# Kernel optimization log

Hardware: AMD Instinct MI355X
Metric: run time of the kernel (lower is better)

## Reference

```python
import jax, jax.numpy as jnp
import numpy as np

B, N, D = 32, 2048, 128
HALF = D // 2
DT = 0.01  # interval = [0.0, 0.01], euler solver -> single step of size 0.01


def setup_inputs() -> dict:
    key = jax.random.key(0)
    ks = jax.random.split(key, 10)
    x = jax.random.normal(ks[0], (B, N, D), dtype=jnp.float32)
    hz = jax.random.normal(ks[1], (B, N, D), dtype=jnp.float32)
    # row-normalized random adjacency so adj @ h stays O(1) (avoids tanh saturation)
    adj = jax.random.uniform(ks[2], (N, N), dtype=jnp.float32) / N
    W1 = jax.random.normal(ks[3], (D, D), dtype=jnp.float32) * 0.05
    W2 = jax.random.normal(ks[4], (D, D), dtype=jnp.float32) * 0.05
    Wa = jax.random.normal(ks[5], (2 * D, 2 * D), dtype=jnp.float32) * 0.05
    ba = jnp.zeros((2 * D,), dtype=jnp.float32)
    Wb = jax.random.normal(ks[6], (2 * D, D), dtype=jnp.float32) * 0.05
    bb = jnp.zeros((D,), dtype=jnp.float32)
    # nn.Parameter init is zeros in torch; randomize in [0,0.1] for a nontrivial baseline
    eps = jax.random.uniform(ks[7], (B, N, HALF), dtype=jnp.float32) * 0.1
    return {"x": x, "hz": hz, "adj": adj, "W1": W1, "W2": W2,
            "Wa": Wa, "ba": ba, "Wb": Wb, "bb": bb, "eps": eps}


def reference(x, hz, adj, W1, W2, Wa, ba, Wb, bb, eps):
    # MLP gating: Linear(2D,2D) -> ReLU -> Linear(2D,D) -> Tanh
    u = jnp.concatenate([x, hz], axis=-1)            # [B,N,2D]
    h = jnp.tanh(jax.nn.relu(u @ Wa + ba) @ Wb + bb)  # [B,N,D]

    def gnn_func(h, W):
        # f(t, h) = tanh(A @ h @ W)  (graph diffusion ODE func)
        return jnp.tanh(jnp.einsum('nm,bmd->bnd', adj, h) @ W)

    def euler_step(h, W):
        # odeint(euler, t=[0, 0.01]): one step y1 = y0 + dt * f(0, y0)
        return h + DT * gnn_func(h, W)

    eps_c = jnp.clip(eps, 0.0, 0.1)
    for _ in range(2):
        h_f = euler_step(h, W1)[..., :HALF]                      # [B,N,D/2]
        h = jnp.concatenate([h_f, h[..., HALF:]], axis=-1)       # [B,N,D]
        h_s = eps_c * euler_step(h, W2)[..., HALF:]              # [B,N,D/2]
        h = jnp.concatenate([h_f, h_s], axis=-1)                 # [B,N,D]
    return h
```

## Files before the change

### kernel.cpp

```cpp
#include <hip/hip_runtime.h>


typedef unsigned short u16;
typedef unsigned int   u32;
typedef unsigned long long u64;
typedef __attribute__((ext_vector_type(8))) short bf8;
typedef __attribute__((ext_vector_type(4))) float f4;

#define AS1 __attribute__((address_space(1)))
#define AS3 __attribute__((address_space(3)))

__device__ __forceinline__ void gl_lds16(const void* g, void* l) {
  __builtin_amdgcn_global_load_lds((const AS1 u32*)g, (AS3 u32*)l, 16, 0, 0);
}
__device__ __forceinline__ float bf2f(u16 v) {
  u32 u = ((u32)v) << 16; return __builtin_bit_cast(float, u);
}
__device__ __forceinline__ u16 f2bf(float f) {
  u32 u = __builtin_bit_cast(u32, f);
  return (u16)((u + 0x7fffu + ((u >> 16) & 1u)) >> 16);
}
__device__ __forceinline__ float ldf(const void* p, size_t i, u32 isf32) {
  return isf32 ? ((const float*)p)[i] : bf2f(((const u16*)p)[i]);
}

__device__ __forceinline__ void stage128x32(const u16* grow0, int stride, u16* lds,
                                            int wave, int lane) {
  int r0 = wave * 16 + (lane >> 2);
  int c0 = (lane & 3) * 8;
  gl_lds16(grow0 + (size_t)r0 * stride + c0, lds + wave * 512);
  gl_lds16(grow0 + (size_t)(64 + r0) * stride + c0, lds + 2048 + wave * 512);
}
__device__ __forceinline__ void stage64x32(const u16* grow0, int stride, u16* lds,
                                           int wave, int lane) {
  gl_lds16(grow0 + (size_t)(wave * 16 + (lane >> 2)) * stride + (lane & 3) * 8,
           lds + wave * 512);
}

__global__ void detect_dtype(const u16* __restrict__ x_raw, u32* __restrict__ flag) {
  __shared__ int s;
  int tid = threadIdx.x;
  if (tid == 0) s = 0;
  __syncthreads();
  int huge = 0;
#pragma unroll
  for (int j = 0; j < 16; ++j) {
    u16 v = x_raw[tid * 16 + j];
    u32 e = (v >> 7) & 0xFF;
    if (e >= 0xC0) huge = 1;
  }
  if (huge) atomicOr(&s, 1);
  __syncthreads();
  if (tid == 0) flag[0] = (u32)s;
}

__global__ void cvt_bf16(const void* __restrict__ in, u16* __restrict__ out,
                         long in_off, int n, const u32* __restrict__ flag) {
  u32 isf32 = flag[0];
  int gid = blockIdx.x * 256 + threadIdx.x;
  long i = in_off + (long)gid * 4;
  if (gid * 4 >= n) return;
  u16 o0, o1, o2, o3;
  if (isf32) {
    f4 v = *(const f4*)&((const float*)in)[i];
    o0 = f2bf(v[0]); o1 = f2bf(v[1]); o2 = f2bf(v[2]); o3 = f2bf(v[3]);
  } else {
    u64 v = *(const u64*)&((const u16*)in)[i];
    o0 = (u16)v; o1 = (u16)(v >> 16); o2 = (u16)(v >> 32); o3 = (u16)(v >> 48);
  }
  u64 pk = (u64)o0 | ((u64)o1 << 16) | ((u64)o2 << 32) | ((u64)o3 << 48);
  *(u64*)&out[(size_t)gid * 4] = pk;
}

__global__ void prep_weights(const void* __restrict__ Wa, const void* __restrict__ Wb,
                             const void* __restrict__ W1, const void* __restrict__ W2,
                             u16* __restrict__ WaT, u16* __restrict__ WbT,
                             u16* __restrict__ W1T, u16* __restrict__ W2T,
                             const u32* __restrict__ flag) {
  u32 isf32 = flag[0];
  int i = blockIdx.x * 256 + threadIdx.x;
  if (i < 65536) {
    int o = i >> 8, k = i & 255; WaT[o * 256 + k] = f2bf(ldf(Wa, (size_t)k * 256 + o, isf32));
  } else if (i < 98304) {
    int j = i - 65536; int o = j >> 8, k = j & 255;
    WbT[o * 256 + k] = f2bf(ldf(Wb, (size_t)k * 128 + o, isf32));
  } else if (i < 106496) {
    int j = i - 98304; int jj = j >> 7, k = j & 127;
    W1T[jj * 128 + k] = f2bf(ldf(W1, (size_t)k * 128 + jj, isf32));
  } else {
    int j = i - 106496; int jj = j >> 7, k = j & 127;
    W2T[jj * 128 + k] = f2bf(ldf(W2, (size_t)k * 128 + 64 + jj, isf32));
  }
}

__global__ __launch_bounds__(256, 2) void mlp_fused(const void* __restrict__ x,
                                                    const void* __restrict__ hz,
                                                    const u16* __restrict__ WaT,
                                                    const void* __restrict__ ba,
                                                    const u16* __restrict__ WbT,
                                                    const void* __restrict__ bb,
                                                    const u16* __restrict__ W1T,
                                                    u16* __restrict__ hT,
                                                    u16* __restrict__ hW,
                                                    const u32* __restrict__ flag) {
  __shared__ __align__(16) u16 Z[64 * 264];
  __shared__ __align__(16) u16 pool[10240];
  u16* lA = pool;
  u16* lB = pool + 2048;
  u16* hN = pool;
  u32 isf32 = flag[0];
  int tid = threadIdx.x, lane = tid & 63, wave = tid >> 6;
  int col = lane & 15, quad = lane >> 4;
  int r0 = blockIdx.x * 64;
  int b = r0 >> 11;

  f4 acc[4][4] = {};
  for (int kk = 0; kk < 8; ++kk) {
    int k0 = kk * 32;
    const void* src = (kk < 4) ? x : hz;
    int csrc = (kk < 4) ? k0 : (k0 - 128);
    __syncthreads();
    {
      int row = tid >> 2, c0 = (tid & 3) * 8;
      size_t g = (size_t)(r0 + row) * 128 + csrc + c0;
      uint4 pk;
      if (isf32) {
        f4 v0 = *(const f4*)&((const float*)src)[g];
        f4 v1 = *(const f4*)&((const float*)src)[g + 4];
        pk.x = (u32)f2bf(v0[0]) | ((u32)f2bf(v0[1]) << 16);
        pk.y = (u32)f2bf(v0[2]) | ((u32)f2bf(v0[3]) << 16);
        pk.z = (u32)f2bf(v1[0]) | ((u32)f2bf(v1[1]) << 16);
        pk.w = (u32)f2bf(v1[2]) | ((u32)f2bf(v1[3]) << 16);
      } else {
        pk = *(const uint4*)&((const u16*)src)[g];
      }
      *(uint4*)&lA[row * 32 + c0] = pk;
    }
    stage128x32(WaT + k0, 256, lB, wave, lane);
    stage128x32(WaT + (size_t)128 * 256 + k0, 256, lB + 4096, wave, lane);
    __syncthreads();
    bf8 af[4], bfr[4];
#pragma unroll
    for (int mi = 0; mi < 4; ++mi) af[mi] = *(const bf8*)&lA[(mi * 16 + col) * 32 + quad * 8];
#pragma unroll
    for (int nj = 0; nj < 4; ++nj) bfr[nj] = *(const bf8*)&lB[(wave * 64 + nj * 16 + col) * 32 + quad * 8];
#pragma unroll
    for (int mi = 0; mi < 4; ++mi)
#pragma unroll
      for (int nj = 0; nj < 4; ++nj)
        acc[mi][nj] = __builtin_amdgcn_mfma_f32_16x16x32_bf16(af[mi], bfr[nj], acc[mi][nj], 0, 0, 0);
  }
#pragma unroll
  for (int mi = 0; mi < 4; ++mi)
#pragma unroll
    for (int nj = 0; nj < 4; ++nj) {
      int o = wave * 64 + nj * 16 + col;
      float bav = ldf(ba, o, isf32);
      int rl = mi * 16 + quad * 4;
#pragma unroll
      for (int r = 0; r < 4; ++r)
        Z[(rl + r) * 264 + o] = f2bf(fmaxf(acc[mi][nj][r] + bav, 0.f));
    }
  __syncthreads();

  f4 acc2[4][2] = {};
  for (int kk = 0; kk < 8; ++kk) {
    int k0 = kk * 32;
    if (kk) __syncthreads();
    stage128x32(WbT + k0, 256, lB, wave, lane);
    __syncthreads();
    bf8 az[4], bw[2];
#pragma unroll
    for (int mi = 0; mi < 4; ++mi) az[mi] = *(const bf8*)&Z[(mi * 16 + col) * 264 + k0 + quad * 8];
#pragma unroll
    for (int nj = 0; nj < 2; ++nj) bw[nj] = *(const bf8*)&lB[(wave * 32 + nj * 16 + col) * 32 + quad * 8];
#pragma unroll
    for (int mi = 0; mi < 4; ++mi)
#pragma unroll
      for (int nj = 0; nj < 2; ++nj)
        acc2[mi][nj] = __builtin_amdgcn_mfma_f32_16x16x32_bf16(az[mi], bw[nj], acc2[mi][nj], 0, 0, 0);
  }
  __syncthreads();

#pragma unroll
  for (int mi = 0; mi < 4; ++mi)
#pragma unroll
    for (int nj = 0; nj < 2; ++nj) {
      int d = wave * 32 + nj * 16 + col;
      float bbv = ldf(bb, d, isf32);
      int rl = mi * 16 + quad * 4;
      int rabs = r0 + rl;
      int n = rabs & 2047;
      u16 p[4];
#pragma unroll
      for (int r = 0; r < 4; ++r) {
        p[r] = f2bf(tanhf(acc2[mi][nj][r] + bbv));
        hN[(rl + r) * 136 + d] = p[r];
      }
      u64 pk = (u64)p[0] | ((u64)p[1] << 16) | ((u64)p[2] << 32) | ((u64)p[3] << 48);
      *(u64*)&hT[(size_t)(b * 128 + d) * 2048 + n] = pk;
    }
  __syncthreads();

  f4 acc3[4] = {};
#pragma unroll
  for (int ks = 0; ks < 4; ++ks) {
    bf8 aw[4], bg;
#pragma unroll
    for (int mi = 0; mi < 4; ++mi)
      aw[mi] = *(const bf8*)&W1T[(size_t)(mi * 16 + col) * 128 + ks * 32 + quad * 8];
    bg = *(const bf8*)&hN[(wave * 16 + col) * 136 + ks * 32 + quad * 8];
#pragma unroll
    for (int mi = 0; mi < 4; ++mi)
      acc3[mi] = __builtin_amdgcn_mfma_f32_16x16x32_bf16(aw[mi], bg, acc3[mi], 0, 0, 0);
  }
#pragma unroll
  for (int mi = 0; mi < 4; ++mi) {
    int rloc = wave * 16 + col;
    int ng = (r0 & 2047) + rloc;
#pragma unroll
    for (int r = 0; r < 4; ++r) {
      int j = mi * 16 + quad * 4 + r;
      hW[(size_t)(b * 64 + j) * 2048 + ng] = f2bf(acc3[mi][r]);
    }
  }
}

__global__ __launch_bounds__(256, 2) void fused_step2(const u16* __restrict__ hin,
                                                      const u16* __restrict__ hWT,
                                                      const u16* __restrict__ adjb,
                                                      const u16* __restrict__ WnT,
                                                      const void* __restrict__ eps,
                                                      u16* __restrict__ hout,
                                                      u16* __restrict__ hWout,
                                                      int half, const u32* __restrict__ flag) {
  __shared__ __align__(16) u16 smem[24576];
  u16* lA = smem;
  u16* lB = smem + 8192;
  u16* gN = smem;
  u32 isf32 = flag[0];
  int tid = threadIdx.x, lane = tid & 63, wave = tid >> 6;
  int col = lane & 15, quad = lane >> 4;
  int b = blockIdx.y;
  int n0 = blockIdx.x * 128;

  const u16* Arow = hWT + (size_t)(b * 64) * 2048;
  const u16* Brow = adjb + (size_t)n0 * 2048;

  f4 acc[4][2] = {};
  for (int kk = 0; kk < 16; ++kk) {
    int k0 = kk * 128;
#pragma unroll
    for (int p = 0; p < 4; ++p) {
      stage64x32(Arow + k0 + p * 32, 2048, lA + p * 2048, wave, lane);
      stage128x32(Brow + k0 + p * 32, 2048, lB + p * 4096, wave, lane);
    }
    __syncthreads();
#pragma unroll
    for (int p = 0; p < 4; ++p) {
      bf8 af[4], bfr[2];
#pragma unroll
      for (int mi = 0; mi < 4; ++mi) af[mi] = *(const bf8*)&lA[p * 2048 + (mi * 16 + col) * 32 + quad * 8];
#pragma unroll
      for (int nj = 0; nj < 2; ++nj) bfr[nj] = *(const bf8*)&lB[p * 4096 + (wave * 32 + nj * 16 + col) * 32 + quad * 8];
#pragma unroll
      for (int mi = 0; mi < 4; ++mi)
#pragma unroll
        for (int nj = 0; nj < 2; ++nj)
          acc[mi][nj] = __builtin_amdgcn_mfma_f32_16x16x32_bf16(af[mi], bfr[nj], acc[mi][nj], 0, 0, 0);
    }
    __syncthreads();
  }

  bool has_eps = (eps != nullptr);
  bool mk_hw = (WnT != nullptr);
  int dBase = half * 64;
#pragma unroll
  for (int mi = 0; mi < 4; ++mi)
#pragma unroll
    for (int nj = 0; nj < 2; ++nj) {
      int j0 = mi * 16 + quad * 4;
      int nl = wave * 32 + nj * 16 + col;
      int n = n0 + nl;
      float ev[4];
      if (has_eps) {
        size_t eoff = ((size_t)b * 2048 + n) * 64 + j0;
        if (isf32) {
          f4 e = *(const f4*)&((const float*)eps)[eoff];
          ev[0] = e[0]; ev[1] = e[1]; ev[2] = e[2]; ev[3] = e[3];
        } else {
          u64 e = *(const u64*)&((const u16*)eps)[eoff];
          ev[0] = bf2f((u16)e); ev[1] = bf2f((u16)(e >> 16));
          ev[2] = bf2f((u16)(e >> 32)); ev[3] = bf2f((u16)(e >> 48));
        }
      }
      u16 pv[4];
#pragma unroll
      for (int r = 0; r < 4; ++r) {
        int j = j0 + r;
        size_t idx = (size_t)(b * 128 + dBase + j) * 2048 + n;
        float hold = bf2f(hin[idx]);
        float nh = hold + 0.01f * tanhf(acc[mi][nj][r]);
        if (has_eps) {
          float e = fminf(fmaxf(ev[r], 0.f), 0.1f);
          nh = e * nh;
        }
        pv[r] = f2bf(nh);
        hout[idx] = pv[r];
      }
      if (mk_hw) {
        u64 pk = (u64)pv[0] | ((u64)pv[1] << 16) | ((u64)pv[2] << 32) | ((u64)pv[3] << 48);
        *(u64*)&gN[nl * 136 + dBase + j0] = pk;
      }
    }

  {
    int oh = (1 - half) * 64;
    const u16* src = hin + (size_t)(b * 128 + oh) * 2048 + n0;
    u16* dst = hout + (size_t)(b * 128 + oh) * 2048 + n0;
#pragma unroll
    for (int i = 0; i < 4; ++i) {
      int idx = i * 256 + tid;
      int rr = idx >> 4;
      int cc = (idx & 15) * 8;
      uint4 v = *(const uint4*)&src[(size_t)rr * 2048 + cc];
      *(uint4*)&dst[(size_t)rr * 2048 + cc] = v;
      if (mk_hw) {
        u16 t[8];
        *(uint4*)t = v;
#pragma unroll
        for (int q = 0; q < 8; ++q) gN[(cc + q) * 136 + oh + rr] = t[q];
      }
    }
  }

  if (mk_hw) {
    __syncthreads();
    f4 acc2[4][2] = {};
#pragma unroll
    for (int ks = 0; ks < 4; ++ks) {
      bf8 aw[4], bg[2];
#pragma unroll
      for (int mi = 0; mi < 4; ++mi)
        aw[mi] = *(const bf8*)&WnT[(size_t)(mi * 16 + col) * 128 + ks * 32 + quad * 8];
#pragma unroll
      for (int nj = 0; nj < 2; ++nj)
        bg[nj] = *(const bf8*)&gN[(wave * 32 + nj * 16 + col) * 136 + ks * 32 + quad * 8];
#pragma unroll
      for (int mi = 0; mi < 4; ++mi)
#pragma unroll
        for (int nj = 0; nj < 2; ++nj)
          acc2[mi][nj] = __builtin_amdgcn_mfma_f32_16x16x32_bf16(aw[mi], bg[nj], acc2[mi][nj], 0, 0, 0);
    }
#pragma unroll
    for (int mi = 0; mi < 4; ++mi)
#pragma unroll
      for (int nj = 0; nj < 2; ++nj) {
        int jp0 = mi * 16 + quad * 4;
        int n = n0 + wave * 32 + nj * 16 + col;
#pragma unroll
        for (int r = 0; r < 4; ++r)
          hWout[(size_t)(b * 64 + jp0 + r) * 2048 + n] = f2bf(acc2[mi][nj][r]);
      }
  }
}

__global__ void untranspose(const u16* __restrict__ hT, void* __restrict__ out,
                            const u32* __restrict__ flag) {
  __shared__ __align__(16) u16 t[64][65];
  u32 isf32 = flag[0];
  int b = blockIdx.z, d0 = blockIdx.y * 64, n0 = blockIdx.x * 64;
  int tid = threadIdx.x;
#pragma unroll
  for (int i = 0; i < 16; ++i) {
    int idx = tid + i * 256;
    int r = idx >> 6, c = idx & 63;
    t[r][c] = hT[(size_t)(b * 128 + d0 + r) * 2048 + n0 + c];
  }
  __syncthreads();
#pragma unroll
  for (int i = 0; i < 16; ++i) {
    int idx = tid + i * 256;
    int r = idx >> 6, c = idx & 63;
    size_t o = (size_t)(b * 2048 + n0 + r) * 128 + d0 + c;
    if (isf32) ((float*)out)[o] = bf2f(t[c][r]);
    else       ((u16*)out)[o] = t[c][r];
  }
}

extern "C" void kernel_launch(void* const* d_in, const int* in_sizes, int n_in,
                              void* d_out, int out_size, void* d_ws, size_t ws_size,
                              hipStream_t stream) {
  const void* x   = d_in[0];
  const void* hz  = d_in[1];
  const void* adj = d_in[2];
  const void* W1  = d_in[3];
  const void* W2  = d_in[4];
  const void* Wa  = d_in[5];
  const void* ba  = d_in[6];
  const void* Wb  = d_in[7];
  const void* bb  = d_in[8];
  const void* eps = d_in[9];

  char* ws = (char*)d_ws;
  u16* hA   = (u16*)(ws);
  u16* adjb = (u16*)(ws + (17ull << 20));
  u16* hWa  = (u16*)(ws + (26ull << 20));
  u16* hWb  = (u16*)(ws + (35ull << 20));
  u16* WaT  = (u16*)(ws + (44ull << 20));
  u16* WbT  = WaT + 256 * 256;
  u16* W1T  = WbT + 128 * 256;
  u16* W2T  = W1T + 64 * 128;
  u32* flag = (u32*)(W2T + 64 * 128);
  u16* hB   = (u16*)d_out;

  detect_dtype<<<dim3(1), dim3(256), 0, stream>>>((const u16*)x, flag);
  prep_weights<<<dim3(448), dim3(256), 0, stream>>>(Wa, Wb, W1, W2, WaT, WbT, W1T, W2T, flag);
  cvt_bf16<<<dim3(4096), dim3(256), 0, stream>>>(adj, adjb, 0, 4194304, flag);
  mlp_fused<<<dim3(1024), dim3(256), 0, stream>>>(x, hz, WaT, ba, WbT, bb, W1T, hA, hWa, flag);
  fused_step2<<<dim3(16, 32), dim3(256), 0, stream>>>(hA, hWa, adjb, W2T, nullptr, hB, hWb, 0, flag);
  fused_step2<<<dim3(16, 32), dim3(256), 0, stream>>>(hB, hWb, adjb, W1T, eps, hA, hWa, 1, flag);
  fused_step2<<<dim3(16, 32), dim3(256), 0, stream>>>(hA, hWa, adjb, W2T, nullptr, hB, hWb, 0, flag);
  fused_step2<<<dim3(16, 32), dim3(256), 0, stream>>>(hB, hWb, adjb, nullptr, eps, hA, nullptr, 1, flag);
  untranspose<<<dim3(32, 2, 32), dim3(256), 0, stream>>>(hA, d_out, flag);
}
```

Baseline: 348.2 us.

## Double-buffer LDS staging and switch to conflict-free quad-major tile layout

Converts the GEMM main loops in mlp_fused and fused_step2 to double-buffered LDS staging, issuing the next tile's global-to-LDS loads before the current tile's MFMAs so that loads overlap compute and one barrier per iteration is removed. It also changes the staged tile layout to a quad-major arrangement (row within 16 contiguous per k-quad) so MFMA fragment reads from LDS avoid bank conflicts. The fused_step2 K-step shrinks from 128 to 64 to fit two buffers, and mlp_fused's LDS pool doubles. The cost is higher LDS use, which may affect occupancy, and more barriers per unit of K in fused_step2.

```diff
diff --git a/kernel.cpp b/kernel.cpp
--- a/kernel.cpp
+++ b/kernel.cpp
@@ -24,17 +24,16 @@
   return isf32 ? ((const float*)p)[i] : bf2f(((const u16*)p)[i]);
 }
 
-__device__ __forceinline__ void stage128x32(const u16* grow0, int stride, u16* lds,
+__device__ __forceinline__ void stage64x32q(const u16* g, int stride, u16* lds,
                                             int wave, int lane) {
-  int r0 = wave * 16 + (lane >> 2);
-  int c0 = (lane & 3) * 8;
-  gl_lds16(grow0 + (size_t)r0 * stride + c0, lds + wave * 512);
-  gl_lds16(grow0 + (size_t)(64 + r0) * stride + c0, lds + 2048 + wave * 512);
-}
-__device__ __forceinline__ void stage64x32(const u16* grow0, int stride, u16* lds,
-                                           int wave, int lane) {
-  gl_lds16(grow0 + (size_t)(wave * 16 + (lane >> 2)) * stride + (lane & 3) * 8,
+  gl_lds16(g + (size_t)(wave * 16 + (lane & 15)) * stride + (lane >> 4) * 8,
            lds + wave * 512);
+}
+__device__ __forceinline__ void stage128x32q(const u16* g, int stride, u16* lds,
+                                             int wave, int lane) {
+  int r = lane & 15, qk = (lane >> 4) * 8;
+  gl_lds16(g + (size_t)(wave * 16 + r) * stride + qk, lds + wave * 512);
+  gl_lds16(g + (size_t)((wave + 4) * 16 + r) * stride + qk, lds + (wave + 4) * 512);
 }
 
 __global__ void detect_dtype(const u16* __restrict__ x_raw, u32* __restrict__ flag) {
@@ -104,9 +103,7 @@
                                                     u16* __restrict__ hW,
                                                     const u32* __restrict__ flag) {
   __shared__ __align__(16) u16 Z[64 * 264];
-  __shared__ __align__(16) u16 pool[10240];
-  u16* lA = pool;
-  u16* lB = pool + 2048;
+  __shared__ __align__(16) u16 pool[20480];
   u16* hN = pool;
   u32 isf32 = flag[0];
   int tid = threadIdx.x, lane = tid & 63, wave = tid >> 6;
@@ -114,42 +111,74 @@
   int r0 = blockIdx.x * 64;
   int b = r0 >> 11;
 
-  f4 acc[4][4] = {};
-  for (int kk = 0; kk < 8; ++kk) {
+  struct A2 { uint4 a, b; };
+  auto loadA = [&](int kk) -> A2 {
     int k0 = kk * 32;
     const void* src = (kk < 4) ? x : hz;
     int csrc = (kk < 4) ? k0 : (k0 - 128);
-    __syncthreads();
-    {
-      int row = tid >> 2, c0 = (tid & 3) * 8;
-      size_t g = (size_t)(r0 + row) * 128 + csrc + c0;
-      uint4 pk;
-      if (isf32) {
-        f4 v0 = *(const f4*)&((const float*)src)[g];
-        f4 v1 = *(const f4*)&((const float*)src)[g + 4];
-        pk.x = (u32)f2bf(v0[0]) | ((u32)f2bf(v0[1]) << 16);
-        pk.y = (u32)f2bf(v0[2]) | ((u32)f2bf(v0[3]) << 16);
-        pk.z = (u32)f2bf(v1[0]) | ((u32)f2bf(v1[1]) << 16);
-        pk.w = (u32)f2bf(v1[2]) | ((u32)f2bf(v1[3]) << 16);
-      } else {
-        pk = *(const uint4*)&((const u16*)src)[g];
-      }
-      *(uint4*)&lA[row * 32 + c0] = pk;
-    }
-    stage128x32(WaT + k0, 256, lB, wave, lane);
-    stage128x32(WaT + (size_t)128 * 256 + k0, 256, lB + 4096, wave, lane);
-    __syncthreads();
+    int row = tid >> 2, c0 = (tid & 3) * 8;
+    size_t g = (size_t)(r0 + row) * 128 + csrc + c0;
+    A2 v;
+    if (isf32) {
+      v.a = *(const uint4*)&((const float*)src)[g];
+      v.b = *(const uint4*)&((const float*)src)[g + 4];
+    } else {
+      v.a = *(const uint4*)&((const u16*)src)[g];
+    }
+    return v;
+  };
+  auto writeA = [&](int buf, A2 v) {
+    uint4 pk;
+    if (isf32) {
+      f4 v0 = __builtin_bit_cast(f4, v.a), v1 = __builtin_bit_cast(f4, v.b);
+      pk.x = (u32)f2bf(v0[0]) | ((u32)f2bf(v0[1]) << 16);
+      pk.y = (u32)f2bf(v0[2]) | ((u32)f2bf(v0[3]) << 16);
+      pk.z = (u32)f2bf(v1[0]) | ((u32)f2bf(v1[1]) << 16);
+      pk.w = (u32)f2bf(v1[2]) | ((u32)f2bf(v1[3]) << 16);
+    } else {
+      pk = v.a;
+    }
+    int row = tid >> 2;
+    *(uint4*)&pool[buf * 2048 + (row >> 4) * 512 + (tid & 3) * 128 + (row & 15) * 8] = pk;
+  };
+  auto stageB1 = [&](int buf, int kk) {
+    int k0 = kk * 32;
+    u16* lb = pool + 4096 + buf * 8192;
+    stage128x32q(WaT + k0, 256, lb, wave, lane);
+    stage128x32q(WaT + (size_t)128 * 256 + k0, 256, lb + 4096, wave, lane);
+  };
+
+  f4 acc[4][4] = {};
+  {
+    A2 v0 = loadA(0);
+    stageB1(0, 0);
+    writeA(0, v0);
+  }
+  __syncthreads();
+  for (int kk = 0; kk < 8; ++kk) {
+    int cur = kk & 1;
+    A2 nx;
+    if (kk < 7) { nx = loadA(kk + 1); stageB1(cur ^ 1, kk + 1); }
+    const u16* la = pool + cur * 2048;
+    const u16* lb = pool + 4096 + cur * 8192;
     bf8 af[4], bfr[4];
 #pragma unroll
-    for (int mi = 0; mi < 4; ++mi) af[mi] = *(const bf8*)&lA[(mi * 16 + col) * 32 + quad * 8];
-#pragma unroll
-    for (int nj = 0; nj < 4; ++nj) bfr[nj] = *(const bf8*)&lB[(wave * 64 + nj * 16 + col) * 32 + quad * 8];
+    for (int mi = 0; mi < 4; ++mi) af[mi] = *(const bf8*)&la[mi * 512 + quad * 128 + col * 8];
+#pragma unroll
+    for (int nj = 0; nj < 4; ++nj) bfr[nj] = *(const bf8*)&lb[(wave * 4 + nj) * 512 + quad * 128 + col * 8];
 #pragma unroll
     for (int mi = 0; mi < 4; ++mi)
 #pragma unroll
       for (int nj = 0; nj < 4; ++nj)
         acc[mi][nj] = __builtin_amdgcn_mfma_f32_16x16x32_bf16(af[mi], bfr[nj], acc[mi][nj], 0, 0, 0);
-  }
+    if (kk < 7) writeA(cur ^ 1, nx);
+    __syncthreads();
+  }
+
+  auto stageB2 = [&](int buf, int kk) {
+    stage128x32q(WbT + kk * 32, 256, pool + 4096 + buf * 4096, wave, lane);
+  };
+  stageB2(0, 0);
 #pragma unroll
   for (int mi = 0; mi < 4; ++mi)
 #pragma unroll
@@ -165,22 +194,22 @@
 
   f4 acc2[4][2] = {};
   for (int kk = 0; kk < 8; ++kk) {
+    int cur = kk & 1;
+    if (kk < 7) stageB2(cur ^ 1, kk + 1);
     int k0 = kk * 32;
-    if (kk) __syncthreads();
-    stage128x32(WbT + k0, 256, lB, wave, lane);
-    __syncthreads();
+    const u16* lb = pool + 4096 + cur * 4096;
     bf8 az[4], bw[2];
 #pragma unroll
     for (int mi = 0; mi < 4; ++mi) az[mi] = *(const bf8*)&Z[(mi * 16 + col) * 264 + k0 + quad * 8];
 #pragma unroll
-    for (int nj = 0; nj < 2; ++nj) bw[nj] = *(const bf8*)&lB[(wave * 32 + nj * 16 + col) * 32 + quad * 8];
+    for (int nj = 0; nj < 2; ++nj) bw[nj] = *(const bf8*)&lb[(wave * 2 + nj) * 512 + quad * 128 + col * 8];
 #pragma unroll
     for (int mi = 0; mi < 4; ++mi)
 #pragma unroll
       for (int nj = 0; nj < 2; ++nj)
         acc2[mi][nj] = __builtin_amdgcn_mfma_f32_16x16x32_bf16(az[mi], bw[nj], acc2[mi][nj], 0, 0, 0);
-  }
-  __syncthreads();
+    __syncthreads();
+  }
 
 #pragma unroll
   for (int mi = 0; mi < 4; ++mi)
@@ -235,8 +264,6 @@
                                                       u16* __restrict__ hWout,
                                                       int half, const u32* __restrict__ flag) {
   __shared__ __align__(16) u16 smem[24576];
-  u16* lA = smem;
-  u16* lB = smem + 8192;
   u16* gN = smem;
   u32 isf32 = flag[0];
   int tid = threadIdx.x, lane = tid & 63, wave = tid >> 6;
@@ -247,22 +274,36 @@
   const u16* Arow = hWT + (size_t)(b * 64) * 2048;
   const u16* Brow = adjb + (size_t)n0 * 2048;
 
+  auto STAGE = [&](int buf, int t) {
+    int k0 = t * 64;
+    u16* la = smem + buf * 4096;
+    u16* lb = smem + 8192 + buf * 8192;
+#pragma unroll
+    for (int p = 0; p < 2; ++p) {
+      int kp = k0 + p * 32;
+      stage64x32q(Arow + kp, 2048, la + p * 2048, wave, lane);
+      stage128x32q(Brow + kp, 2048, lb + p * 4096, wave, lane);
+    }
+  };
+
   f4 acc[4][2] = {};
-  for (int kk = 0; kk < 16; ++kk) {
-    int k0 = kk * 128;
-#pragma unroll
-    for (int p = 0; p < 4; ++p) {
-      stage64x32(Arow + k0 + p * 32, 2048, lA + p * 2048, wave, lane);
-      stage128x32(Brow + k0 + p * 32, 2048, lB + p * 4096, wave, lane);
-    }
-    __syncthreads();
-#pragma unroll
-    for (int p = 0; p < 4; ++p) {
+  STAGE(0, 0);
+  __syncthreads();
+#pragma unroll 2
+  for (int kk = 0; kk < 32; ++kk) {
+    int cur = kk & 1;
+    if (kk < 31) STAGE(cur ^ 1, kk + 1);
+    const u16* la = smem + cur * 4096;
+    const u16* lb = smem + 8192 + cur * 8192;
+#pragma unroll
+    for (int p = 0; p < 2; ++p) {
       bf8 af[4], bfr[2];
 #pragma unroll
-      for (int mi = 0; mi < 4; ++mi) af[mi] = *(const bf8*)&lA[p * 2048 + (mi * 16 + col) * 32 + quad * 8];
-#pragma unroll
-      for (int nj = 0; nj < 2; ++nj) bfr[nj] = *(const bf8*)&lB[p * 4096 + (wave * 32 + nj * 16 + col) * 32 + quad * 8];
+      for (int mi = 0; mi < 4; ++mi)
+        af[mi] = *(const bf8*)&la[p * 2048 + mi * 512 + quad * 128 + col * 8];
+#pragma unroll
+      for (int nj = 0; nj < 2; ++nj)
+        bfr[nj] = *(const bf8*)&lb[p * 4096 + (wave * 2 + nj) * 512 + quad * 128 + col * 8];
 #pragma unroll
       for (int mi = 0; mi < 4; ++mi)
 #pragma unroll
```

New measurement: 443.7 us. 27.4% more time.

## Triple-buffer async LDS staging with vmcnt waits in MLP and graph GEMM kernels

Applied to the files above, without the earlier changes.

Replaces the load-then-compute loops in mlp_fused and fused_step2 with a three-stage ring of LDS buffers. Global-to-LDS loads are issued two steps ahead and gated by s_waitcnt vmcnt plus a raw barrier, and MFMA sections are raised with s_setprio. The activation tile is preloaded whole, and staging switches to a quad-major LDS layout. This is meant to hide global memory latency behind MFMA work, at the cost of more LDS per block, which may lower occupancy, and fragile hand-counted wait values.

```diff
diff --git a/kernel.cpp b/kernel.cpp
--- a/kernel.cpp
+++ b/kernel.cpp
@@ -9,6 +9,8 @@
 
 #define AS1 __attribute__((address_space(1)))
 #define AS3 __attribute__((address_space(3)))
+#define WAITVM(N) asm volatile("s_waitcnt vmcnt(" #N ")" ::: "memory")
+#define BARS __builtin_amdgcn_s_barrier()
 
 __device__ __forceinline__ void gl_lds16(const void* g, void* l) {
   __builtin_amdgcn_global_load_lds((const AS1 u32*)g, (AS3 u32*)l, 16, 0, 0);
@@ -24,17 +26,16 @@
   return isf32 ? ((const float*)p)[i] : bf2f(((const u16*)p)[i]);
 }
 
-__device__ __forceinline__ void stage128x32(const u16* grow0, int stride, u16* lds,
+__device__ __forceinline__ void stage64x32q(const u16* g, int stride, u16* lds,
                                             int wave, int lane) {
-  int r0 = wave * 16 + (lane >> 2);
-  int c0 = (lane & 3) * 8;
-  gl_lds16(grow0 + (size_t)r0 * stride + c0, lds + wave * 512);
-  gl_lds16(grow0 + (size_t)(64 + r0) * stride + c0, lds + 2048 + wave * 512);
-}
-__device__ __forceinline__ void stage64x32(const u16* grow0, int stride, u16* lds,
-                                           int wave, int lane) {
-  gl_lds16(grow0 + (size_t)(wave * 16 + (lane >> 2)) * stride + (lane & 3) * 8,
+  gl_lds16(g + (size_t)(wave * 16 + (lane & 15)) * stride + (lane >> 4) * 8,
            lds + wave * 512);
+}
+__device__ __forceinline__ void stage128x32q(const u16* g, int stride, u16* lds,
+                                             int wave, int lane) {
+  int r = lane & 15, qk = (lane >> 4) * 8;
+  gl_lds16(g + (size_t)(wave * 16 + r) * stride + qk, lds + wave * 512);
+  gl_lds16(g + (size_t)((wave + 4) * 16 + r) * stride + qk, lds + (wave + 4) * 512);
 }
 
 __global__ void detect_dtype(const u16* __restrict__ x_raw, u32* __restrict__ flag) {
@@ -103,26 +104,53 @@
                                                     u16* __restrict__ hT,
                                                     u16* __restrict__ hW,
                                                     const u32* __restrict__ flag) {
-  __shared__ __align__(16) u16 Z[64 * 264];
-  __shared__ __align__(16) u16 pool[10240];
-  u16* lA = pool;
-  u16* lB = pool + 2048;
-  u16* hN = pool;
+  __shared__ __align__(16) u16 smem[40960];
+  u16* Afull = smem;
+  u16* Zp = smem + 16384;
+  u16* hN = smem;
   u32 isf32 = flag[0];
   int tid = threadIdx.x, lane = tid & 63, wave = tid >> 6;
   int col = lane & 15, quad = lane >> 4;
   int r0 = blockIdx.x * 64;
   int b = r0 >> 11;
 
+  auto stageB1 = [&](int buf, int kk) {
+    u16* lb = smem + 16384 + buf * 8192;
+    stage128x32q(WaT + kk * 32, 256, lb, wave, lane);
+    stage128x32q(WaT + (size_t)128 * 256 + kk * 32, 256, lb + 4096, wave, lane);
+  };
+  auto stageB2 = [&](int buf, int kk) {
+    stage128x32q(WbT + kk * 32, 256, smem + buf * 4096, wave, lane);
+  };
+
   f4 acc[4][4] = {};
-  for (int kk = 0; kk < 8; ++kk) {
-    int k0 = kk * 32;
-    const void* src = (kk < 4) ? x : hz;
-    int csrc = (kk < 4) ? k0 : (k0 - 128);
-    __syncthreads();
-    {
-      int row = tid >> 2, c0 = (tid & 3) * 8;
-      size_t g = (size_t)(r0 + row) * 128 + csrc + c0;
+  auto P1 = [&](int buf, int kk) {
+    const u16* lb = smem + 16384 + buf * 8192;
+    bf8 af[4], bfr[4];
+#pragma unroll
+    for (int mi = 0; mi < 4; ++mi)
+      af[mi] = *(const bf8*)&Afull[kk * 2048 + mi * 512 + quad * 128 + col * 8];
+#pragma unroll
+    for (int nj = 0; nj < 4; ++nj)
+      bfr[nj] = *(const bf8*)&lb[(wave * 4 + nj) * 512 + quad * 128 + col * 8];
+    __builtin_amdgcn_s_setprio(1);
+#pragma unroll
+    for (int mi = 0; mi < 4; ++mi)
+#pragma unroll
+      for (int nj = 0; nj < 4; ++nj)
+        acc[mi][nj] = __builtin_amdgcn_mfma_f32_16x16x32_bf16(af[mi], bfr[nj], acc[mi][nj], 0, 0, 0);
+    __builtin_amdgcn_s_setprio(0);
+  };
+
+  stageB1(0, 0); stageB1(1, 1);
+  {
+    int r = ((tid >> 6) << 4) | (tid & 15);
+    int c0 = ((tid >> 4) & 3) * 8;
+#pragma unroll
+    for (int kk = 0; kk < 8; ++kk) {
+      const void* src = (kk < 4) ? x : hz;
+      int cc = (kk & 3) * 32 + c0;
+      size_t g = (size_t)(r0 + r) * 128 + cc;
       uint4 pk;
       if (isf32) {
         f4 v0 = *(const f4*)&((const float*)src)[g];
@@ -134,22 +162,22 @@
       } else {
         pk = *(const uint4*)&((const u16*)src)[g];
       }
-      *(uint4*)&lA[row * 32 + c0] = pk;
-    }
-    stage128x32(WaT + k0, 256, lB, wave, lane);
-    stage128x32(WaT + (size_t)128 * 256 + k0, 256, lB + 4096, wave, lane);
-    __syncthreads();
-    bf8 af[4], bfr[4];
-#pragma unroll
-    for (int mi = 0; mi < 4; ++mi) af[mi] = *(const bf8*)&lA[(mi * 16 + col) * 32 + quad * 8];
-#pragma unroll
-    for (int nj = 0; nj < 4; ++nj) bfr[nj] = *(const bf8*)&lB[(wave * 64 + nj * 16 + col) * 32 + quad * 8];
-#pragma unroll
-    for (int mi = 0; mi < 4; ++mi)
-#pragma unroll
-      for (int nj = 0; nj < 4; ++nj)
-        acc[mi][nj] = __builtin_amdgcn_mfma_f32_16x16x32_bf16(af[mi], bfr[nj], acc[mi][nj], 0, 0, 0);
-  }
+      *(uint4*)&Afull[kk * 2048 + tid * 8] = pk;
+    }
+  }
+  __syncthreads();
+
+#pragma unroll 1
+  for (int kk0 = 0; kk0 < 6; kk0 += 3) {
+    WAITVM(4); BARS; stageB1(2, kk0 + 2); P1(0, kk0);
+    WAITVM(4); BARS; stageB1(0, kk0 + 3); P1(1, kk0 + 1);
+    WAITVM(4); BARS; stageB1(1, kk0 + 4); P1(2, kk0 + 2);
+  }
+  WAITVM(4); BARS; P1(0, 6);
+  WAITVM(0); BARS; P1(1, 7);
+  __syncthreads();
+
+  stageB2(0, 0); stageB2(1, 1);
 #pragma unroll
   for (int mi = 0; mi < 4; ++mi)
 #pragma unroll
@@ -159,27 +187,37 @@
       int rl = mi * 16 + quad * 4;
 #pragma unroll
       for (int r = 0; r < 4; ++r)
-        Z[(rl + r) * 264 + o] = f2bf(fmaxf(acc[mi][nj][r] + bav, 0.f));
-    }
-  __syncthreads();
+        Zp[(rl + r) * 264 + o] = f2bf(fmaxf(acc[mi][nj][r] + bav, 0.f));
+    }
+  asm volatile("s_waitcnt lgkmcnt(0)" ::: "memory");
+  BARS;
 
   f4 acc2[4][2] = {};
-  for (int kk = 0; kk < 8; ++kk) {
-    int k0 = kk * 32;
-    if (kk) __syncthreads();
-    stage128x32(WbT + k0, 256, lB, wave, lane);
-    __syncthreads();
+  auto P2 = [&](int buf, int kk) {
+    const u16* lb = smem + buf * 4096;
     bf8 az[4], bw[2];
 #pragma unroll
-    for (int mi = 0; mi < 4; ++mi) az[mi] = *(const bf8*)&Z[(mi * 16 + col) * 264 + k0 + quad * 8];
-#pragma unroll
-    for (int nj = 0; nj < 2; ++nj) bw[nj] = *(const bf8*)&lB[(wave * 32 + nj * 16 + col) * 32 + quad * 8];
+    for (int mi = 0; mi < 4; ++mi)
+      az[mi] = *(const bf8*)&Zp[(mi * 16 + col) * 264 + kk * 32 + quad * 8];
+#pragma unroll
+    for (int nj = 0; nj < 2; ++nj)
+      bw[nj] = *(const bf8*)&lb[(wave * 2 + nj) * 512 + quad * 128 + col * 8];
+    __builtin_amdgcn_s_setprio(1);
 #pragma unroll
     for (int mi = 0; mi < 4; ++mi)
 #pragma unroll
       for (int nj = 0; nj < 2; ++nj)
         acc2[mi][nj] = __builtin_amdgcn_mfma_f32_16x16x32_bf16(az[mi], bw[nj], acc2[mi][nj], 0, 0, 0);
-  }
+    __builtin_amdgcn_s_setprio(0);
+  };
+#pragma unroll 1
+  for (int kk0 = 0; kk0 < 6; kk0 += 3) {
+    WAITVM(2); BARS; stageB2(2, kk0 + 2); P2(0, kk0);
+    WAITVM(2); BARS; stageB2(0, kk0 + 3); P2(1, kk0 + 1);
+    WAITVM(2); BARS; stageB2(1, kk0 + 4); P2(2, kk0 + 2);
+  }
+  WAITVM(2); BARS; P2(0, 6);
+  WAITVM(0); BARS; P2(1, 7);
   __syncthreads();
 
 #pragma unroll
@@ -234,9 +272,7 @@
                                                       u16* __restrict__ hout,
                                                       u16* __restrict__ hWout,
                                                       int half, const u32* __restrict__ flag) {
-  __shared__ __align__(16) u16 smem[24576];
-  u16* lA = smem;
-  u16* lB = smem + 8192;
+  __shared__ __align__(16) u16 smem[36864];
   u16* gN = smem;
   u32 isf32 = flag[0];
   int tid = threadIdx.x, lane = tid & 63, wave = tid >> 6;
@@ -247,30 +283,52 @@
   const u16* Arow = hWT + (size_t)(b * 64) * 2048;
   const u16* Brow = adjb + (size_t)n0 * 2048;
 
+  auto STAGE = [&](int buf, int t) {
+    int k0 = t * 64;
+    u16* la = smem + buf * 12288;
+    u16* lb = la + 4096;
+#pragma unroll
+    for (int p = 0; p < 2; ++p) {
+      stage64x32q(Arow + k0 + p * 32, 2048, la + p * 2048, wave, lane);
+      stage128x32q(Brow + k0 + p * 32, 2048, lb + p * 4096, wave, lane);
+    }
+  };
+
   f4 acc[4][2] = {};
-  for (int kk = 0; kk < 16; ++kk) {
-    int k0 = kk * 128;
-#pragma unroll
-    for (int p = 0; p < 4; ++p) {
-      stage64x32(Arow + k0 + p * 32, 2048, lA + p * 2048, wave, lane);
-      stage128x32(Brow + k0 + p * 32, 2048, lB + p * 4096, wave, lane);
-    }
-    __syncthreads();
-#pragma unroll
-    for (int p = 0; p < 4; ++p) {
-      bf8 af[4], bfr[2];
-#pragma unroll
-      for (int mi = 0; mi < 4; ++mi) af[mi] = *(const bf8*)&lA[p * 2048 + (mi * 16 + col) * 32 + quad * 8];
-#pragma unroll
-      for (int nj = 0; nj < 2; ++nj) bfr[nj] = *(const bf8*)&lB[p * 4096 + (wave * 32 + nj * 16 + col) * 32 + quad * 8];
+  auto COMP = [&](int buf) {
+    const u16* la = smem + buf * 12288;
+    const u16* lb = la + 4096;
+    bf8 af[2][4], bfr[2][2];
+#pragma unroll
+    for (int p = 0; p < 2; ++p) {
 #pragma unroll
       for (int mi = 0; mi < 4; ++mi)
+        af[p][mi] = *(const bf8*)&la[p * 2048 + mi * 512 + quad * 128 + col * 8];
+#pragma unroll
+      for (int nj = 0; nj < 2; ++nj)
+        bfr[p][nj] = *(const bf8*)&lb[p * 4096 + (wave * 2 + nj) * 512 + quad * 128 + col * 8];
+    }
+    __builtin_amdgcn_s_setprio(1);
+#pragma unroll
+    for (int p = 0; p < 2; ++p)
+#pragma unroll
+      for (int mi = 0; mi < 4; ++mi)
 #pragma unroll
         for (int nj = 0; nj < 2; ++nj)
-          acc[mi][nj] = __builtin_amdgcn_mfma_f32_16x16x32_bf16(af[mi], bfr[nj], acc[mi][nj], 0, 0, 0);
-    }
-    __syncthreads();
-  }
+          acc[mi][nj] = __builtin_amdgcn_mfma_f32_16x16x32_bf16(af[p][mi], bfr[p][nj], acc[mi][nj], 0, 0, 0);
+    __builtin_amdgcn_s_setprio(0);
+  };
+
+  STAGE(0, 0); STAGE(1, 1);
+#pragma unroll 1
+  for (int kk0 = 0; kk0 < 30; kk0 += 3) {
+    WAITVM(6); BARS; STAGE(2, kk0 + 2); COMP(0);
+    WAITVM(6); BARS; STAGE(0, kk0 + 3); COMP(1);
+    WAITVM(6); BARS; STAGE(1, kk0 + 4); COMP(2);
+  }
+  WAITVM(6); BARS; COMP(0);
+  WAITVM(0); BARS; COMP(1);
+  __syncthreads();
 
   bool has_eps = (eps != nullptr);
   bool mk_hw = (WnT != nullptr);
```

New measurement: 432.5 us. 1.24x slower.

## Load GEMM operands directly from global into registers with register double-buffering

Applied to the files above, without the earlier changes.

Drops LDS staging through global_load_lds in the adjacency GEMM and the MLP weight GEMMs. MFMA fragments are now loaded straight from global memory into registers, with a two-deep software pipeline and no block barriers in the main loops. The grid order is swapped so consecutive blocks share the adjacency rows via L2, and launch bounds are raised to 4 blocks per SM for occupancy. The cost is that each wave now issues its own uncoalesced 16-byte row loads, with no cross-wave sharing of A and B tiles, which raises L2 traffic.

```diff
diff --git a/kernel.cpp b/kernel.cpp
--- a/kernel.cpp
+++ b/kernel.cpp
@@ -7,12 +7,6 @@
 typedef __attribute__((ext_vector_type(8))) short bf8;
 typedef __attribute__((ext_vector_type(4))) float f4;
 
-#define AS1 __attribute__((address_space(1)))
-#define AS3 __attribute__((address_space(3)))
-
-__device__ __forceinline__ void gl_lds16(const void* g, void* l) {
-  __builtin_amdgcn_global_load_lds((const AS1 u32*)g, (AS3 u32*)l, 16, 0, 0);
-}
 __device__ __forceinline__ float bf2f(u16 v) {
   u32 u = ((u32)v) << 16; return __builtin_bit_cast(float, u);
 }
@@ -22,19 +16,6 @@
 }
 __device__ __forceinline__ float ldf(const void* p, size_t i, u32 isf32) {
   return isf32 ? ((const float*)p)[i] : bf2f(((const u16*)p)[i]);
-}
-
-__device__ __forceinline__ void stage128x32(const u16* grow0, int stride, u16* lds,
-                                            int wave, int lane) {
-  int r0 = wave * 16 + (lane >> 2);
-  int c0 = (lane & 3) * 8;
-  gl_lds16(grow0 + (size_t)r0 * stride + c0, lds + wave * 512);
-  gl_lds16(grow0 + (size_t)(64 + r0) * stride + c0, lds + 2048 + wave * 512);
-}
-__device__ __forceinline__ void stage64x32(const u16* grow0, int stride, u16* lds,
-                                           int wave, int lane) {
-  gl_lds16(grow0 + (size_t)(wave * 16 + (lane >> 2)) * stride + (lane & 3) * 8,
-           lds + wave * 512);
 }
 
 __global__ void detect_dtype(const u16* __restrict__ x_raw, u32* __restrict__ flag) {
@@ -103,26 +84,23 @@
                                                     u16* __restrict__ hT,
                                                     u16* __restrict__ hW,
                                                     const u32* __restrict__ flag) {
+  __shared__ __align__(16) u16 Afull[16384];
   __shared__ __align__(16) u16 Z[64 * 264];
-  __shared__ __align__(16) u16 pool[10240];
-  u16* lA = pool;
-  u16* lB = pool + 2048;
-  u16* hN = pool;
+  u16* hN = Afull;
   u32 isf32 = flag[0];
   int tid = threadIdx.x, lane = tid & 63, wave = tid >> 6;
   int col = lane & 15, quad = lane >> 4;
   int r0 = blockIdx.x * 64;
   int b = r0 >> 11;
 
-  f4 acc[4][4] = {};
-  for (int kk = 0; kk < 8; ++kk) {
-    int k0 = kk * 32;
-    const void* src = (kk < 4) ? x : hz;
-    int csrc = (kk < 4) ? k0 : (k0 - 128);
-    __syncthreads();
-    {
-      int row = tid >> 2, c0 = (tid & 3) * 8;
-      size_t g = (size_t)(r0 + row) * 128 + csrc + c0;
+  {
+    int r = ((tid >> 6) << 4) | (tid & 15);
+    int c0 = ((tid >> 4) & 3) * 8;
+#pragma unroll
+    for (int kk = 0; kk < 8; ++kk) {
+      const void* src = (kk < 4) ? x : hz;
+      int cc = (kk & 3) * 32 + c0;
+      size_t g = (size_t)(r0 + r) * 128 + cc;
       uint4 pk;
       if (isf32) {
         f4 v0 = *(const f4*)&((const float*)src)[g];
@@ -134,21 +112,38 @@
       } else {
         pk = *(const uint4*)&((const u16*)src)[g];
       }
-      *(uint4*)&lA[row * 32 + c0] = pk;
-    }
-    stage128x32(WaT + k0, 256, lB, wave, lane);
-    stage128x32(WaT + (size_t)128 * 256 + k0, 256, lB + 4096, wave, lane);
-    __syncthreads();
-    bf8 af[4], bfr[4];
-#pragma unroll
-    for (int mi = 0; mi < 4; ++mi) af[mi] = *(const bf8*)&lA[(mi * 16 + col) * 32 + quad * 8];
-#pragma unroll
-    for (int nj = 0; nj < 4; ++nj) bfr[nj] = *(const bf8*)&lB[(wave * 64 + nj * 16 + col) * 32 + quad * 8];
-#pragma unroll
-    for (int mi = 0; mi < 4; ++mi)
-#pragma unroll
-      for (int nj = 0; nj < 4; ++nj)
-        acc[mi][nj] = __builtin_amdgcn_mfma_f32_16x16x32_bf16(af[mi], bfr[nj], acc[mi][nj], 0, 0, 0);
+      *(uint4*)&Afull[kk * 2048 + tid * 8] = pk;
+    }
+  }
+  __syncthreads();
+
+  f4 acc[4][4] = {};
+  {
+    const u16* Wrow = WaT + (size_t)(wave * 64 + col) * 256 + quad * 8;
+    bf8 bc[4], bn[4];
+#pragma unroll
+    for (int nj = 0; nj < 4; ++nj) bc[nj] = *(const bf8*)&Wrow[(size_t)nj * 16 * 256];
+#pragma unroll
+    for (int kk = 0; kk < 8; ++kk) {
+      if (kk < 7) {
+#pragma unroll
+        for (int nj = 0; nj < 4; ++nj)
+          bn[nj] = *(const bf8*)&Wrow[(size_t)nj * 16 * 256 + (kk + 1) * 32];
+      }
+      bf8 af[4];
+#pragma unroll
+      for (int mi = 0; mi < 4; ++mi)
+        af[mi] = *(const bf8*)&Afull[kk * 2048 + mi * 512 + quad * 128 + col * 8];
+#pragma unroll
+      for (int mi = 0; mi < 4; ++mi)
+#pragma unroll
+        for (int nj = 0; nj < 4; ++nj)
+          acc[mi][nj] = __builtin_amdgcn_mfma_f32_16x16x32_bf16(af[mi], bc[nj], acc[mi][nj], 0, 0, 0);
+      if (kk < 7) {
+#pragma unroll
+        for (int nj = 0; nj < 4; ++nj) bc[nj] = bn[nj];
+      }
+    }
   }
 #pragma unroll
   for (int mi = 0; mi < 4; ++mi)
@@ -164,21 +159,32 @@
   __syncthreads();
 
   f4 acc2[4][2] = {};
-  for (int kk = 0; kk < 8; ++kk) {
-    int k0 = kk * 32;
-    if (kk) __syncthreads();
-    stage128x32(WbT + k0, 256, lB, wave, lane);
-    __syncthreads();
-    bf8 az[4], bw[2];
-#pragma unroll
-    for (int mi = 0; mi < 4; ++mi) az[mi] = *(const bf8*)&Z[(mi * 16 + col) * 264 + k0 + quad * 8];
-#pragma unroll
-    for (int nj = 0; nj < 2; ++nj) bw[nj] = *(const bf8*)&lB[(wave * 32 + nj * 16 + col) * 32 + quad * 8];
-#pragma unroll
-    for (int mi = 0; mi < 4; ++mi)
-#pragma unroll
-      for (int nj = 0; nj < 2; ++nj)
-        acc2[mi][nj] = __builtin_amdgcn_mfma_f32_16x16x32_bf16(az[mi], bw[nj], acc2[mi][nj], 0, 0, 0);
+  {
+    const u16* Wrow = WbT + (size_t)(wave * 32 + col) * 256 + quad * 8;
+    bf8 bc[2], bn[2];
+#pragma unroll
+    for (int nj = 0; nj < 2; ++nj) bc[nj] = *(const bf8*)&Wrow[(size_t)nj * 16 * 256];
+#pragma unroll
+    for (int kk = 0; kk < 8; ++kk) {
+      if (kk < 7) {
+#pragma unroll
+        for (int nj = 0; nj < 2; ++nj)
+          bn[nj] = *(const bf8*)&Wrow[(size_t)nj * 16 * 256 + (kk + 1) * 32];
+      }
+      bf8 az[4];
+#pragma unroll
+      for (int mi = 0; mi < 4; ++mi)
+        az[mi] = *(const bf8*)&Z[(mi * 16 + col) * 264 + kk * 32 + quad * 8];
+#pragma unroll
+      for (int mi = 0; mi < 4; ++mi)
+#pragma unroll
+        for (int nj = 0; nj < 2; ++nj)
+          acc2[mi][nj] = __builtin_amdgcn_mfma_f32_16x16x32_bf16(az[mi], bc[nj], acc2[mi][nj], 0, 0, 0);
+      if (kk < 7) {
+#pragma unroll
+        for (int nj = 0; nj < 2; ++nj) bc[nj] = bn[nj];
+      }
+    }
   }
   __syncthreads();
 
@@ -226,7 +232,7 @@
   }
 }
 
-__global__ __launch_bounds__(256, 2) void fused_step2(const u16* __restrict__ hin,
+__global__ __launch_bounds__(256, 4) void fused_step2(const u16* __restrict__ hin,
                                                       const u16* __restrict__ hWT,
                                                       const u16* __restrict__ adjb,
                                                       const u16* __restrict__ WnT,
@@ -234,43 +240,55 @@
                                                       u16* __restrict__ hout,
                                                       u16* __restrict__ hWout,
                                                       int half, const u32* __restrict__ flag) {
-  __shared__ __align__(16) u16 smem[24576];
-  u16* lA = smem;
-  u16* lB = smem + 8192;
-  u16* gN = smem;
+  __shared__ __align__(16) u16 gN[128 * 136];
   u32 isf32 = flag[0];
   int tid = threadIdx.x, lane = tid & 63, wave = tid >> 6;
   int col = lane & 15, quad = lane >> 4;
-  int b = blockIdx.y;
-  int n0 = blockIdx.x * 128;
-
-  const u16* Arow = hWT + (size_t)(b * 64) * 2048;
-  const u16* Brow = adjb + (size_t)n0 * 2048;
-
+  int b = blockIdx.x;
+  int n0 = blockIdx.y * 128;
+
+  const u16* Ab = hWT + (size_t)(b * 64 + col) * 2048 + quad * 8;
+  const u16* Bb = adjb + (size_t)(n0 + wave * 32 + col) * 2048 + quad * 8;
+
+  bf8 a0[4], b0[2], a1[4], b1[2];
   f4 acc[4][2] = {};
-  for (int kk = 0; kk < 16; ++kk) {
-    int k0 = kk * 128;
-#pragma unroll
-    for (int p = 0; p < 4; ++p) {
-      stage64x32(Arow + k0 + p * 32, 2048, lA + p * 2048, wave, lane);
-      stage128x32(Brow + k0 + p * 32, 2048, lB + p * 4096, wave, lane);
-    }
-    __syncthreads();
-#pragma unroll
-    for (int p = 0; p < 4; ++p) {
-      bf8 af[4], bfr[2];
-#pragma unroll
-      for (int mi = 0; mi < 4; ++mi) af[mi] = *(const bf8*)&lA[p * 2048 + (mi * 16 + col) * 32 + quad * 8];
-#pragma unroll
-      for (int nj = 0; nj < 2; ++nj) bfr[nj] = *(const bf8*)&lB[p * 4096 + (wave * 32 + nj * 16 + col) * 32 + quad * 8];
-#pragma unroll
-      for (int mi = 0; mi < 4; ++mi)
-#pragma unroll
-        for (int nj = 0; nj < 2; ++nj)
-          acc[mi][nj] = __builtin_amdgcn_mfma_f32_16x16x32_bf16(af[mi], bfr[nj], acc[mi][nj], 0, 0, 0);
-    }
-    __syncthreads();
-  }
+
+#define LA(t, dst)                                                         \
+  {                                                                        \
+    _Pragma("unroll")                                                      \
+    for (int mi = 0; mi < 4; ++mi)                                         \
+      dst[mi] = *(const bf8*)&Ab[(size_t)mi * 16 * 2048 + (t) * 32];       \
+  }
+#define LB(t, dst)                                                         \
+  {                                                                        \
+    _Pragma("unroll")                                                      \
+    for (int nj = 0; nj < 2; ++nj)                                         \
+      dst[nj] = *(const bf8*)&Bb[(size_t)nj * 16 * 2048 + (t) * 32];       \
+  }
+#define MM(af, bf)                                                         \
+  {                                                                        \
+    _Pragma("unroll")                                                      \
+    for (int mi = 0; mi < 4; ++mi)                                         \
+      _Pragma("unroll")                                                    \
+      for (int nj = 0; nj < 2; ++nj)                                       \
+        acc[mi][nj] = __builtin_amdgcn_mfma_f32_16x16x32_bf16(             \
+            af[mi], bf[nj], acc[mi][nj], 0, 0, 0);                         \
+  }
+
+  LA(0, a0); LB(0, b0);
+#pragma unroll 1
+  for (int t = 0; t < 62; t += 2) {
+    LA(t + 1, a1); LB(t + 1, b1);
+    MM(a0, b0);
+    LA(t + 2, a0); LB(t + 2, b0);
+    MM(a1, b1);
+  }
+  LA(63, a1); LB(63, b1);
+  MM(a0, b0);
+  MM(a1, b1);
+#undef LA
+#undef LB
+#undef MM
 
   bool has_eps = (eps != nullptr);
   bool mk_hw = (WnT != nullptr);
@@ -418,9 +436,9 @@
   prep_weights<<<dim3(448), dim3(256), 0, stream>>>(Wa, Wb, W1, W2, WaT, WbT, W1T, W2T, flag);
   cvt_bf16<<<dim3(4096), dim3(256), 0, stream>>>(adj, adjb, 0, 4194304, flag);
   mlp_fused<<<dim3(1024), dim3(256), 0, stream>>>(x, hz, WaT, ba, WbT, bb, W1T, hA, hWa, flag);
-  fused_step2<<<dim3(16, 32), dim3(256), 0, stream>>>(hA, hWa, adjb, W2T, nullptr, hB, hWb, 0, flag);
-  fused_step2<<<dim3(16, 32), dim3(256), 0, stream>>>(hB, hWb, adjb, W1T, eps, hA, hWa, 1, flag);
-  fused_step2<<<dim3(16, 32), dim3(256), 0, stream>>>(hA, hWa, adjb, W2T, nullptr, hB, hWb, 0, flag);
-  fused_step2<<<dim3(16, 32), dim3(256), 0, stream>>>(hB, hWb, adjb, nullptr, eps, hA, nullptr, 1, flag);
+  fused_step2<<<dim3(32, 16), dim3(256), 0, stream>>>(hA, hWa, adjb, W2T, nullptr, hB, hWb, 0, flag);
+  fused_step2<<<dim3(32, 16), dim3(256), 0, stream>>>(hB, hWb, adjb, W1T, eps, hA, hWa, 1, flag);
+  fused_step2<<<dim3(32, 16), dim3(256), 0, stream>>>(hA, hWa, adjb, W2T, nullptr, hB, hWb, 0, flag);
+  fused_step2<<<dim3(32, 16), dim3(256), 0, stream>>>(hB, hWb, adjb, nullptr, eps, hA, nullptr, 1, flag);
   untranspose<<<dim3(32, 2, 32), dim3(256), 0, stream>>>(hA, d_out, flag);
 }
```

After: 600.4 us. 72.4% more time.
